# Kernel tuning notes

Measured on AMD Instinct MI355X. Metric: run time of the kernel, lower is better.

Reference implementation:

```python
import jax, jax.numpy as jnp
import numpy as np

B, H, D, DV, N, M = 1, 8, 64, 64, 2048, 128


def setup_inputs() -> dict:
    key = jax.random.key(0)
    k1, k2, k3, k4 = jax.random.split(key, 4)
    keys = jax.random.normal(k1, (B, H, D, N), dtype=jnp.float32)
    values = jax.random.normal(k2, (B, H, DV, N), dtype=jnp.float32)
    queries = jax.random.normal(k3, (B, H, D, N), dtype=jnp.float32)
    # orthonormal random features: QR of (m, key_dim) gaussian (reduced QR, m >= key_dim)
    raw = np.asarray(jax.random.normal(k4, (M, D), dtype=jnp.float32), dtype=np.float64)
    features = jnp.asarray(np.linalg.qr(raw)[0], dtype=jnp.float32)  # (M, D)
    return {"keys": keys, "values": values, "queries": queries, "features": features}


def reference(keys, values, queries, features):
    b, h, d, n = keys.shape
    dv = values.shape[2]
    m = features.shape[0]
    phi_scale = 1.0 / jnp.sqrt(jnp.asarray(m, keys.dtype))
    # flatten heads into batch, move locations to axis 1: (B*H, N, D)
    k = keys.reshape(b * h, d, n).transpose(0, 2, 1)
    v = values.reshape(b * h, dv, n).transpose(0, 2, 1)
    q = queries.reshape(b * h, d, n).transpose(0, 2, 1)

    def phi(x):  # (BH, N, D) -> (BH, N, M); f=[relu], h(x)=1.0
        return jax.nn.relu(jnp.einsum('bnd,md->bnm', x, features)) * phi_scale

    phi_k = phi(k)
    phi_q = phi(q)
    # causal linear attention: prefix sums of phi_k (x) v outer products
    kv = jnp.cumsum(phi_k[:, :, :, None] * v[:, :, None, :], axis=1)  # (BH, N, M, DV)
    out = jnp.einsum('bnm,bnmv->bnv', phi_q, kv)                      # (BH, N, DV)
    norm = jnp.einsum('bnm,bnm->bn', phi_q, jnp.cumsum(phi_k, axis=1))
    out = out / norm[:, :, None]
    out = out.transpose(0, 2, 1).reshape(b, h, dv, n)
    return out
```

## Files before the change

### kernel.cpp

```cpp
#include <hip/hip_runtime.h>


#define BH 8
#define D 64
#define DV 64
#define NSEQ 2048
#define M 128
#define CHK 64
#define NC (NSEQ / CHK)
#define PHI_SCALE 0.08838834764831845f

typedef unsigned int uint;
typedef unsigned short ushort;
typedef __attribute__((ext_vector_type(8))) short bf16x8;
typedef __attribute__((ext_vector_type(4))) float f32x4;
#define MFMA16(a, b, c) __builtin_amdgcn_mfma_f32_16x16x32_bf16((a), (b), (c), 0, 0, 0)

__device__ __forceinline__ short f2bf(float x) {
    uint u = __float_as_uint(x);
    u += 0x7fffu + ((u >> 16) & 1u);
    return (short)(u >> 16);
}
__device__ __forceinline__ float bf2f(short b) {
    return __uint_as_float(((uint)(ushort)b) << 16);
}

__global__ __launch_bounds__(256) void favor_p1(
    const float* __restrict__ keys, const float* __restrict__ values,
    const float* __restrict__ features, ushort* __restrict__ St,
    float* __restrict__ z)
{
    const int bh = blockIdx.x >> 5, c = blockIdx.x & 31, n0 = c * CHK;
    const int tid = threadIdx.x;
    const int lane = tid & 63, wid = tid >> 6, quad = lane >> 4, l16 = lane & 15;

    __shared__ ulong2 smv[2048];
    short* sF  = (short*)smv;
    short* sPK = (short*)smv + 8192;

    for (int i = tid; i < 8192; i += 256) sF[i] = f2bf(features[i]);
    __syncthreads();

    {
        const float* Kb = keys + bh * D * NSEQ + n0 + 16 * wid + l16;
        bf16x8 bK[2];
        for (int h = 0; h < 2; ++h)
            for (int j = 0; j < 8; ++j)
                bK[h][j] = f2bf(Kb[(32 * h + 8 * quad + j) * NSEQ]);
        for (int mt = 0; mt < 8; ++mt) {
            f32x4 acc = {0.f, 0.f, 0.f, 0.f};
            for (int h = 0; h < 2; ++h) {
                bf16x8 aF = *(const bf16x8*)(sF + (16 * mt + l16) * 64 + 32 * h + 8 * quad);
                acc = MFMA16(aF, bK[h], acc);
            }
            for (int r = 0; r < 4; ++r)
                sPK[(16 * mt + 4 * quad + r) * 64 + 16 * wid + l16] =
                    f2bf(fmaxf(acc[r], 0.f) * PHI_SCALE);
        }
    }
    __syncthreads();

    if (tid < 128) {
        float s = 0.f;
        for (int n = 0; n < 64; ++n) s += bf2f(sPK[tid * 64 + ((n + tid) & 63)]);
        z[(bh * NC + c) * M + tid] = s;
    }

    {
        const float* Vb = values + bh * DV * NSEQ + n0;
        bf16x8 aV[2];
        for (int h = 0; h < 2; ++h) {
            const float4* vp = (const float4*)(Vb + (16 * wid + l16) * NSEQ + 32 * h + 8 * quad);
            float4 v0 = vp[0], v1 = vp[1];
            aV[h][0] = f2bf(v0.x); aV[h][1] = f2bf(v0.y);
            aV[h][2] = f2bf(v0.z); aV[h][3] = f2bf(v0.w);
            aV[h][4] = f2bf(v1.x); aV[h][5] = f2bf(v1.y);
            aV[h][6] = f2bf(v1.z); aV[h][7] = f2bf(v1.w);
        }
        ushort* So = St + (size_t)(bh * NC + c) * (DV * M);
        for (int mt = 0; mt < 8; ++mt) {
            f32x4 acc = {0.f, 0.f, 0.f, 0.f};
            for (int h = 0; h < 2; ++h) {
                bf16x8 bP = *(const bf16x8*)(sPK + (16 * mt + l16) * 64 + 32 * h + 8 * quad);
                acc = MFMA16(aV[h], bP, acc);
            }
            for (int r = 0; r < 4; ++r)
                So[(16 * wid + 4 * quad + r) * M + 16 * mt + l16] = (ushort)f2bf(acc[r]);
        }
    }
}

__global__ __launch_bounds__(256) void favor_p2(ushort* __restrict__ St,
                                                float* __restrict__ z)
{
    const int gid = blockIdx.x * 256 + threadIdx.x;
    if (blockIdx.x < 256) {
        const int bh = gid >> 13, vm = gid & 8191;
        ushort* p = St + (size_t)bh * NC * 8192 + vm;
        float vals[NC];
        #pragma unroll
        for (int cc = 0; cc < NC; ++cc) vals[cc] = bf2f(p[cc * 8192]);
        float run = 0.f;
        #pragma unroll
        for (int cc = 0; cc < NC; ++cc) { p[cc * 8192] = (ushort)f2bf(run); run += vals[cc]; }
    } else {
        const int i = gid - 65536;
        if (i < BH * M) {
            const int bh = i >> 7, m = i & 127;
            float* p = z + bh * NC * M + m;
            float vals[NC];
            #pragma unroll
            for (int cc = 0; cc < NC; ++cc) vals[cc] = p[cc * M];
            float run = 0.f;
            #pragma unroll
            for (int cc = 0; cc < NC; ++cc) { p[cc * M] = run; run += vals[cc]; }
        }
    }
}

__global__ __launch_bounds__(256) void favor_p3(
    const float* __restrict__ keys, const float* __restrict__ values,
    const float* __restrict__ queries, const ushort* __restrict__ St,
    const float* __restrict__ z, const float* __restrict__ features,
    float* __restrict__ out)
{
    const int bh = blockIdx.x >> 5, c = blockIdx.x & 31, n0 = c * CHK;
    const int tid = threadIdx.x;
    const int lane = tid & 63, wid = tid >> 6, quad = lane >> 4, l16 = lane & 15;

    __shared__ ulong2 smv[3120];
    char* sm = (char*)smv;
    short* sF   = (short*)sm;
    short* sAm  = (short*)sm;
    short* sV   = (short*)(sm + 8192);
    short* sPQ  = (short*)(sm + 16384);
    float* sOut = (float*)(sm + 16384);
    short* sPK  = (short*)(sm + 32768);
    float* sZ   = (float*)(sm + 49152);
    float* sNm  = (float*)(sm + 49664);

    for (int i = tid; i < 8192; i += 256) sF[i] = f2bf(features[i]);
    if (tid < 128) sZ[tid] = z[(bh * NC + c) * M + tid];
    __syncthreads();

    {
        const float* Qb = queries + bh * D * NSEQ + n0 + 16 * wid + l16;
        const float* Kb = keys    + bh * D * NSEQ + n0 + 16 * wid + l16;
        bf16x8 aQ[2], aK[2];
        for (int h = 0; h < 2; ++h)
            for (int j = 0; j < 8; ++j) {
                const int d = 32 * h + 8 * quad + j;
                aQ[h][j] = f2bf(Qb[d * NSEQ]);
                aK[h][j] = f2bf(Kb[d * NSEQ]);
            }
        for (int mt = 0; mt < 8; ++mt) {
            f32x4 accQ = {0.f, 0.f, 0.f, 0.f}, accK = {0.f, 0.f, 0.f, 0.f};
            for (int h = 0; h < 2; ++h) {
                bf16x8 bF = *(const bf16x8*)(sF + (16 * mt + l16) * 64 + 32 * h + 8 * quad);
                accQ = MFMA16(aQ[h], bF, accQ);
                accK = MFMA16(aK[h], bF, accK);
            }
            for (int r = 0; r < 4; ++r) {
                const int row = (16 * wid + 4 * quad + r) * M + 16 * mt + l16;
                sPQ[row] = f2bf(fmaxf(accQ[r], 0.f) * PHI_SCALE);
                sPK[row] = f2bf(fmaxf(accK[r], 0.f) * PHI_SCALE);
            }
        }
    }
    __syncthreads();

    f32x4 accO[4], accC[4];
    for (int t = 0; t < 4; ++t) { accO[t] = (f32x4){0.f,0.f,0.f,0.f}; accC[t] = (f32x4){0.f,0.f,0.f,0.f}; }
    {
        const ushort* Sb = St + (size_t)(bh * NC + c) * (DV * M);
        for (int mt = 0; mt < 4; ++mt) {
            bf16x8 aP = *(const bf16x8*)(sPQ + (16 * wid + l16) * M + 32 * mt + 8 * quad);
            for (int vt = 0; vt < 4; ++vt) {
                bf16x8 bS = *(const bf16x8*)(Sb + (16 * vt + l16) * M + 32 * mt + 8 * quad);
                accO[vt] = MFMA16(aP, bS, accO[vt]);
            }
            for (int jt = 0; jt < 4; ++jt) {
                bf16x8 bK2 = *(const bf16x8*)(sPK + (16 * jt + l16) * M + 32 * mt + 8 * quad);
                accC[jt] = MFMA16(aP, bK2, accC[jt]);
            }
        }
    }
    float rsum[4] = {0.f, 0.f, 0.f, 0.f};
    for (int jt = 0; jt < 4; ++jt)
        for (int r = 0; r < 4; ++r) {
            const int n = 16 * wid + 4 * quad + r;
            const int j = 16 * jt + l16;
            const float av = (j <= n) ? accC[jt][r] : 0.f;
            rsum[r] += av;
            sAm[n * 64 + j] = f2bf(av);
        }
    for (int r = 0; r < 4; ++r) {
        float s = rsum[r];
        s += __shfl_xor(s, 1); s += __shfl_xor(s, 2);
        s += __shfl_xor(s, 4); s += __shfl_xor(s, 8);
        if (l16 == 0) sNm[16 * wid + 4 * quad + r] = s;
    }
    __syncthreads();

    for (int i = tid; i < 4096; i += 256) {
        const int v = i >> 6, j = i & 63;
        sV[v * 64 + j] = f2bf(values[(bh * DV + v) * NSEQ + n0 + j]);
    }
    if (tid < 64) {
        float s = 0.f;
        for (int mm = 0; mm < 128; ++mm) {
            const int m = (mm + 2 * tid) & 127;
            s += bf2f(sPQ[tid * M + m]) * sZ[m];
        }
        sNm[tid] += s;
    }
    __syncthreads();

    for (int jh = 0; jh < 2; ++jh) {
        bf16x8 aA = *(const bf16x8*)(sAm + (16 * wid + l16) * 64 + 32 * jh + 8 * quad);
        for (int vt = 0; vt < 4; ++vt) {
            bf16x8 bV = *(const bf16x8*)(sV + (16 * vt + l16) * 64 + 32 * jh + 8 * quad);
            accO[vt] = MFMA16(aA, bV, accO[vt]);
        }
    }
    for (int vt = 0; vt < 4; ++vt)
        for (int r = 0; r < 4; ++r) {
            const int n = 16 * wid + 4 * quad + r, v = 16 * vt + l16;
            sOut[n * 65 + v] = accO[vt][r] / sNm[n];
        }
    __syncthreads();

    for (int i = tid; i < 4096; i += 256) {
        const int v = i >> 6, n = i & 63;
        out[(bh * DV + v) * NSEQ + n0 + n] = sOut[n * 65 + v];
    }
}

extern "C" void kernel_launch(void* const* d_in, const int* in_sizes, int n_in,
                              void* d_out, int out_size, void* d_ws, size_t ws_size,
                              hipStream_t stream)
{
    (void)in_sizes; (void)n_in; (void)out_size; (void)ws_size;
    const float* keys     = (const float*)d_in[0];
    const float* values   = (const float*)d_in[1];
    const float* queries  = (const float*)d_in[2];
    const float* features = (const float*)d_in[3];
    float* outp = (float*)d_out;

    ushort* St = (ushort*)d_ws;
    float*  z  = (float*)((char*)d_ws + (size_t)BH * NC * DV * M * sizeof(ushort));

    favor_p1<<<dim3(BH * NC), dim3(256), 0, stream>>>(keys, values, features, St, z);
    favor_p2<<<dim3(260), dim3(256), 0, stream>>>(St, z);
    favor_p3<<<dim3(BH * NC), dim3(256), 0, stream>>>(keys, values, queries, St, z,
                                                      features, outp);
}
```

Measured before the change: 90.47 us.

## Fuse three-phase linear attention into one cooperative kernel with grid syncs

Merges the three kernels (chunk state build, cross-chunk prefix scan, output) into a single cooperative kernel that uses two grid-wide syncs. Keys, queries, values and features are loaded and projected once, and the intra-chunk work is kept in shared memory across the syncs. XOR-swizzled shared-memory layouts are added to reduce bank conflicts. This removes two kernel launches and the duplicated loads and feature projections. In exchange it needs a larger shared-memory footprint (about 82 KB per block) and adds grid-barrier cost, and all 256 blocks must be co-resident.

```diff
diff --git a/kernel.cpp b/kernel.cpp
--- a/kernel.cpp
+++ b/kernel.cpp
@@ -1,4 +1,7 @@
 #include <hip/hip_runtime.h>
+#include <hip/hip_cooperative_groups.h>
+
+namespace cg = cooperative_groups;
 
 
 #define BH 8
@@ -13,6 +16,7 @@
 typedef unsigned int uint;
 typedef unsigned short ushort;
 typedef __attribute__((ext_vector_type(8))) short bf16x8;
+typedef __attribute__((ext_vector_type(4))) short bf16x4;
 typedef __attribute__((ext_vector_type(4))) float f32x4;
 #define MFMA16(a, b, c) __builtin_amdgcn_mfma_f32_16x16x32_bf16((a), (b), (c), 0, 0, 0)
 
@@ -25,50 +29,40 @@
     return __uint_as_float(((uint)(ushort)b) << 16);
 }
 
-__global__ __launch_bounds__(256) void favor_p1(
+#define SWZ64(r, c)  ((r) * 64  + ((c) ^ (((r) & 7) << 3)))
+#define SWZ128(r, c) ((r) * 128 + ((c) ^ (((r) & 7) << 3)))
+
+__global__ __launch_bounds__(256) void favor_fused(
     const float* __restrict__ keys, const float* __restrict__ values,
-    const float* __restrict__ features, ushort* __restrict__ St,
-    float* __restrict__ z)
+    const float* __restrict__ queries, const float* __restrict__ features,
+    ushort* __restrict__ St, float* __restrict__ z, float* __restrict__ out)
 {
     const int bh = blockIdx.x >> 5, c = blockIdx.x & 31, n0 = c * CHK;
     const int tid = threadIdx.x;
     const int lane = tid & 63, wid = tid >> 6, quad = lane >> 4, l16 = lane & 15;
 
-    __shared__ ulong2 smv[2048];
-    short* sF  = (short*)smv;
-    short* sPK = (short*)smv + 8192;
-
-    for (int i = tid; i < 8192; i += 256) sF[i] = f2bf(features[i]);
-    __syncthreads();
-
-    {
-        const float* Kb = keys + bh * D * NSEQ + n0 + 16 * wid + l16;
-        bf16x8 bK[2];
-        for (int h = 0; h < 2; ++h)
-            for (int j = 0; j < 8; ++j)
-                bK[h][j] = f2bf(Kb[(32 * h + 8 * quad + j) * NSEQ]);
-        for (int mt = 0; mt < 8; ++mt) {
-            f32x4 acc = {0.f, 0.f, 0.f, 0.f};
-            for (int h = 0; h < 2; ++h) {
-                bf16x8 aF = *(const bf16x8*)(sF + (16 * mt + l16) * 64 + 32 * h + 8 * quad);
-                acc = MFMA16(aF, bK[h], acc);
-            }
-            for (int r = 0; r < 4; ++r)
-                sPK[(16 * mt + 4 * quad + r) * 64 + 16 * wid + l16] =
-                    f2bf(fmaxf(acc[r], 0.f) * PHI_SCALE);
-        }
-    }
-    __syncthreads();
-
-    if (tid < 128) {
-        float s = 0.f;
-        for (int n = 0; n < 64; ++n) s += bf2f(sPK[tid * 64 + ((n + tid) & 63)]);
-        z[(bh * NC + c) * M + tid] = s;
-    }
-
+    __shared__ ulong2 smv[5168];
+    short* sF    = (short*)smv;
+    short* sPKmn = (short*)smv + 8192;
+    short* sPQt  = (short*)smv + 16384;
+    short* sPKt  = (short*)smv + 24576;
+    short* sAm   = (short*)smv + 32768;
+    short* sV    = (short*)smv + 36864;
+    float* sNm   = (float*)((char*)smv + 81920);
+    float* sZ    = (float*)((char*)smv + 82176);
+    float* sOut  = (float*)smv;
+
+    const float* Kb = keys    + bh * D * NSEQ + n0 + 16 * wid + l16;
+    const float* Qb = queries + bh * D * NSEQ + n0 + 16 * wid + l16;
+    bf16x8 bK[2], aQ[2], aV[2];
+    for (int h = 0; h < 2; ++h)
+        for (int j = 0; j < 8; ++j) {
+            const int d = 32 * h + 8 * quad + j;
+            bK[h][j] = f2bf(Kb[d * NSEQ]);
+            aQ[h][j] = f2bf(Qb[d * NSEQ]);
+        }
     {
         const float* Vb = values + bh * DV * NSEQ + n0;
-        bf16x8 aV[2];
         for (int h = 0; h < 2; ++h) {
             const float4* vp = (const float4*)(Vb + (16 * wid + l16) * NSEQ + 32 * h + 8 * quad);
             float4 v0 = vp[0], v1 = vp[1];
@@ -77,112 +71,63 @@
             aV[h][4] = f2bf(v1.x); aV[h][5] = f2bf(v1.y);
             aV[h][6] = f2bf(v1.z); aV[h][7] = f2bf(v1.w);
         }
+        for (int h = 0; h < 2; ++h)
+            *(bf16x8*)(sV + SWZ64(16 * wid + l16, 32 * h + 8 * quad)) = aV[h];
+    }
+    for (int k = 0; k < 8; ++k) {
+        const int i = tid + 256 * k;
+        float4 f = ((const float4*)features)[i];
+        const int e = 4 * i, row = e >> 6, col = e & 63;
+        bf16x4 bq;
+        bq[0] = f2bf(f.x); bq[1] = f2bf(f.y); bq[2] = f2bf(f.z); bq[3] = f2bf(f.w);
+        *(bf16x4*)(sF + SWZ64(row, col)) = bq;
+    }
+    __syncthreads();
+
+    for (int mt = 0; mt < 8; ++mt) {
+        f32x4 aMN = {0.f,0.f,0.f,0.f}, aQm = {0.f,0.f,0.f,0.f}, aKm = {0.f,0.f,0.f,0.f};
+        for (int h = 0; h < 2; ++h) {
+            bf16x8 fF = *(const bf16x8*)(sF + SWZ64(16 * mt + l16, 32 * h + 8 * quad));
+            aMN = MFMA16(fF, bK[h], aMN);
+            aQm = MFMA16(aQ[h], fF, aQm);
+            aKm = MFMA16(bK[h], fF, aKm);
+        }
+        for (int r = 0; r < 4; ++r) {
+            const int mr = 16 * mt + 4 * quad + r;
+            sPKmn[SWZ64(mr, 16 * wid + l16)] = f2bf(fmaxf(aMN[r], 0.f) * PHI_SCALE);
+            const int nr = 16 * wid + 4 * quad + r;
+            sPQt[SWZ128(nr, 16 * mt + l16)] = f2bf(fmaxf(aQm[r], 0.f) * PHI_SCALE);
+            sPKt[SWZ128(nr, 16 * mt + l16)] = f2bf(fmaxf(aKm[r], 0.f) * PHI_SCALE);
+        }
+    }
+    __syncthreads();
+
+    if (tid < 128) {
+        float s = 0.f;
+        for (int n = 0; n < 64; ++n) s += bf2f(sPKmn[SWZ64(tid, (n + tid) & 63)]);
+        z[(bh * NC + c) * M + tid] = s;
+    }
+
+    {
         ushort* So = St + (size_t)(bh * NC + c) * (DV * M);
         for (int mt = 0; mt < 8; ++mt) {
-            f32x4 acc = {0.f, 0.f, 0.f, 0.f};
+            f32x4 acc = {0.f,0.f,0.f,0.f};
             for (int h = 0; h < 2; ++h) {
-                bf16x8 bP = *(const bf16x8*)(sPK + (16 * mt + l16) * 64 + 32 * h + 8 * quad);
+                bf16x8 bP = *(const bf16x8*)(sPKmn + SWZ64(16 * mt + l16, 32 * h + 8 * quad));
                 acc = MFMA16(aV[h], bP, acc);
             }
             for (int r = 0; r < 4; ++r)
                 So[(16 * wid + 4 * quad + r) * M + 16 * mt + l16] = (ushort)f2bf(acc[r]);
         }
     }
-}
-
-__global__ __launch_bounds__(256) void favor_p2(ushort* __restrict__ St,
-                                                float* __restrict__ z)
-{
-    const int gid = blockIdx.x * 256 + threadIdx.x;
-    if (blockIdx.x < 256) {
-        const int bh = gid >> 13, vm = gid & 8191;
-        ushort* p = St + (size_t)bh * NC * 8192 + vm;
-        float vals[NC];
-        #pragma unroll
-        for (int cc = 0; cc < NC; ++cc) vals[cc] = bf2f(p[cc * 8192]);
-        float run = 0.f;
-        #pragma unroll
-        for (int cc = 0; cc < NC; ++cc) { p[cc * 8192] = (ushort)f2bf(run); run += vals[cc]; }
-    } else {
-        const int i = gid - 65536;
-        if (i < BH * M) {
-            const int bh = i >> 7, m = i & 127;
-            float* p = z + bh * NC * M + m;
-            float vals[NC];
-            #pragma unroll
-            for (int cc = 0; cc < NC; ++cc) vals[cc] = p[cc * M];
-            float run = 0.f;
-            #pragma unroll
-            for (int cc = 0; cc < NC; ++cc) { p[cc * M] = run; run += vals[cc]; }
-        }
-    }
-}
-
-__global__ __launch_bounds__(256) void favor_p3(
-    const float* __restrict__ keys, const float* __restrict__ values,
-    const float* __restrict__ queries, const ushort* __restrict__ St,
-    const float* __restrict__ z, const float* __restrict__ features,
-    float* __restrict__ out)
-{
-    const int bh = blockIdx.x >> 5, c = blockIdx.x & 31, n0 = c * CHK;
-    const int tid = threadIdx.x;
-    const int lane = tid & 63, wid = tid >> 6, quad = lane >> 4, l16 = lane & 15;
-
-    __shared__ ulong2 smv[3120];
-    char* sm = (char*)smv;
-    short* sF   = (short*)sm;
-    short* sAm  = (short*)sm;
-    short* sV   = (short*)(sm + 8192);
-    short* sPQ  = (short*)(sm + 16384);
-    float* sOut = (float*)(sm + 16384);
-    short* sPK  = (short*)(sm + 32768);
-    float* sZ   = (float*)(sm + 49152);
-    float* sNm  = (float*)(sm + 49664);
-
-    for (int i = tid; i < 8192; i += 256) sF[i] = f2bf(features[i]);
-    if (tid < 128) sZ[tid] = z[(bh * NC + c) * M + tid];
-    __syncthreads();
-
-    {
-        const float* Qb = queries + bh * D * NSEQ + n0 + 16 * wid + l16;
-        const float* Kb = keys    + bh * D * NSEQ + n0 + 16 * wid + l16;
-        bf16x8 aQ[2], aK[2];
-        for (int h = 0; h < 2; ++h)
-            for (int j = 0; j < 8; ++j) {
-                const int d = 32 * h + 8 * quad + j;
-                aQ[h][j] = f2bf(Qb[d * NSEQ]);
-                aK[h][j] = f2bf(Kb[d * NSEQ]);
-            }
-        for (int mt = 0; mt < 8; ++mt) {
-            f32x4 accQ = {0.f, 0.f, 0.f, 0.f}, accK = {0.f, 0.f, 0.f, 0.f};
-            for (int h = 0; h < 2; ++h) {
-                bf16x8 bF = *(const bf16x8*)(sF + (16 * mt + l16) * 64 + 32 * h + 8 * quad);
-                accQ = MFMA16(aQ[h], bF, accQ);
-                accK = MFMA16(aK[h], bF, accK);
-            }
-            for (int r = 0; r < 4; ++r) {
-                const int row = (16 * wid + 4 * quad + r) * M + 16 * mt + l16;
-                sPQ[row] = f2bf(fmaxf(accQ[r], 0.f) * PHI_SCALE);
-                sPK[row] = f2bf(fmaxf(accK[r], 0.f) * PHI_SCALE);
-            }
-        }
-    }
-    __syncthreads();
 
     f32x4 accO[4], accC[4];
     for (int t = 0; t < 4; ++t) { accO[t] = (f32x4){0.f,0.f,0.f,0.f}; accC[t] = (f32x4){0.f,0.f,0.f,0.f}; }
-    {
-        const ushort* Sb = St + (size_t)(bh * NC + c) * (DV * M);
-        for (int mt = 0; mt < 4; ++mt) {
-            bf16x8 aP = *(const bf16x8*)(sPQ + (16 * wid + l16) * M + 32 * mt + 8 * quad);
-            for (int vt = 0; vt < 4; ++vt) {
-                bf16x8 bS = *(const bf16x8*)(Sb + (16 * vt + l16) * M + 32 * mt + 8 * quad);
-                accO[vt] = MFMA16(aP, bS, accO[vt]);
-            }
-            for (int jt = 0; jt < 4; ++jt) {
-                bf16x8 bK2 = *(const bf16x8*)(sPK + (16 * jt + l16) * M + 32 * mt + 8 * quad);
-                accC[jt] = MFMA16(aP, bK2, accC[jt]);
-            }
+    for (int mt = 0; mt < 4; ++mt) {
+        bf16x8 aP = *(const bf16x8*)(sPQt + SWZ128(16 * wid + l16, 32 * mt + 8 * quad));
+        for (int jt = 0; jt < 4; ++jt) {
+            bf16x8 bK2 = *(const bf16x8*)(sPKt + SWZ128(16 * jt + l16, 32 * mt + 8 * quad));
+            accC[jt] = MFMA16(aP, bK2, accC[jt]);
         }
     }
     float rsum[4] = {0.f, 0.f, 0.f, 0.f};
@@ -192,7 +137,7 @@
             const int j = 16 * jt + l16;
             const float av = (j <= n) ? accC[jt][r] : 0.f;
             rsum[r] += av;
-            sAm[n * 64 + j] = f2bf(av);
+            sAm[SWZ64(n, j)] = f2bf(av);
         }
     for (int r = 0; r < 4; ++r) {
         float s = rsum[r];
@@ -202,34 +147,67 @@
     }
     __syncthreads();
 
-    for (int i = tid; i < 4096; i += 256) {
-        const int v = i >> 6, j = i & 63;
-        sV[v * 64 + j] = f2bf(values[(bh * DV + v) * NSEQ + n0 + j]);
-    }
+    for (int jh = 0; jh < 2; ++jh) {
+        bf16x8 aA = *(const bf16x8*)(sAm + SWZ64(16 * wid + l16, 32 * jh + 8 * quad));
+        for (int vt = 0; vt < 4; ++vt) {
+            bf16x8 bV = *(const bf16x8*)(sV + SWZ64(16 * vt + l16, 32 * jh + 8 * quad));
+            accO[vt] = MFMA16(aA, bV, accO[vt]);
+        }
+    }
+
+    cg::this_grid().sync();
+
+    {
+        const int gid = blockIdx.x * 256 + tid;
+        const int sbh = gid >> 13, vm = gid & 8191;
+        ushort* p = St + (size_t)sbh * NC * 8192 + vm;
+        float vals[NC];
+        #pragma unroll
+        for (int cc = 0; cc < NC; ++cc) vals[cc] = bf2f(p[cc * 8192]);
+        float run = 0.f;
+        #pragma unroll
+        for (int cc = 0; cc < NC; ++cc) { p[cc * 8192] = (ushort)f2bf(run); run += vals[cc]; }
+        if (blockIdx.x < 4) {
+            const int i = blockIdx.x * 256 + tid;
+            const int zbh = i >> 7, m = i & 127;
+            float* zp = z + zbh * NC * M + m;
+            #pragma unroll
+            for (int cc = 0; cc < NC; ++cc) vals[cc] = zp[cc * M];
+            float zr = 0.f;
+            #pragma unroll
+            for (int cc = 0; cc < NC; ++cc) { zp[cc * M] = zr; zr += vals[cc]; }
+        }
+    }
+
+    cg::this_grid().sync();
+
+    if (tid < 128) sZ[tid] = z[(bh * NC + c) * M + tid];
+    {
+        const ushort* Sb = St + (size_t)(bh * NC + c) * (DV * M);
+        for (int mt = 0; mt < 4; ++mt) {
+            bf16x8 aP = *(const bf16x8*)(sPQt + SWZ128(16 * wid + l16, 32 * mt + 8 * quad));
+            for (int vt = 0; vt < 4; ++vt) {
+                bf16x8 bS = *(const bf16x8*)(Sb + (16 * vt + l16) * M + 32 * mt + 8 * quad);
+                accO[vt] = MFMA16(aP, bS, accO[vt]);
+            }
+        }
+    }
+    __syncthreads();
     if (tid < 64) {
         float s = 0.f;
         for (int mm = 0; mm < 128; ++mm) {
             const int m = (mm + 2 * tid) & 127;
-            s += bf2f(sPQ[tid * M + m]) * sZ[m];
+            s += bf2f(sPQt[SWZ128(tid, m)]) * sZ[m];
         }
         sNm[tid] += s;
     }
     __syncthreads();
-
-    for (int jh = 0; jh < 2; ++jh) {
-        bf16x8 aA = *(const bf16x8*)(sAm + (16 * wid + l16) * 64 + 32 * jh + 8 * quad);
-        for (int vt = 0; vt < 4; ++vt) {
-            bf16x8 bV = *(const bf16x8*)(sV + (16 * vt + l16) * 64 + 32 * jh + 8 * quad);
-            accO[vt] = MFMA16(aA, bV, accO[vt]);
-        }
-    }
     for (int vt = 0; vt < 4; ++vt)
         for (int r = 0; r < 4; ++r) {
             const int n = 16 * wid + 4 * quad + r, v = 16 * vt + l16;
             sOut[n * 65 + v] = accO[vt][r] / sNm[n];
         }
     __syncthreads();
-
     for (int i = tid; i < 4096; i += 256) {
         const int v = i >> 6, n = i & 63;
         out[(bh * DV + v) * NSEQ + n0 + n] = sOut[n * 65 + v];
@@ -250,8 +228,8 @@
     ushort* St = (ushort*)d_ws;
     float*  z  = (float*)((char*)d_ws + (size_t)BH * NC * DV * M * sizeof(ushort));
 
-    favor_p1<<<dim3(BH * NC), dim3(256), 0, stream>>>(keys, values, features, St, z);
-    favor_p2<<<dim3(260), dim3(256), 0, stream>>>(St, z);
-    favor_p3<<<dim3(BH * NC), dim3(256), 0, stream>>>(keys, values, queries, St, z,
-                                                      features, outp);
-}
+    void* args[] = {(void*)&keys, (void*)&values, (void*)&queries, (void*)&features,
+                    (void*)&St, (void*)&z, (void*)&outp};
+    hipLaunchCooperativeKernel(reinterpret_cast<const void*>(&favor_fused),
+                               dim3(BH * NC), dim3(256), args, 0u, stream);
+}
```

Result: slower. 146.6 us (+62.0%).
